# Performance work log

Hardware: AMD Instinct MI355X
Metric: run time of the kernel (lower is better)

Reference implementation:

```python
import jax, jax.numpy as jnp
import numpy as np

C = 96        # dim
HEADS = 8     # FrameHistoryRouter heads (StateAlignBlock forces heads=1)
WS = 4        # window_size = 2*scale_patchsize
NFC = 1       # num_frames_tocache
TOPK = 5
LOCAL_N = 4


def conv(x, w, stride=1, pad=0, groups=1):
    return jax.lax.conv_general_dilated(
        x, w, (stride, stride), [(pad, pad), (pad, pad)],
        dimension_numbers=("NCHW", "OIHW", "NCHW"), feature_group_count=groups)


def l2norm(x, axis):
    n = jnp.linalg.norm(x, axis=axis, keepdims=True)
    return x / jnp.maximum(n, 1e-12)


def setup_inputs() -> dict:
    key = jax.random.key(0)
    ks = jax.random.split(key, 16)
    def rn(i, shp, s=0.02):
        return jax.random.normal(ks[i], shp, dtype=jnp.float32) * s
    return {
        "x": jax.random.normal(ks[0], (2, C, 256, 256), dtype=jnp.float32),
        "sab_qk_w": rn(1, (2 * C, C, 1, 1)),
        "sab_qk_dw": rn(2, (2 * C, 1, 3, 3)),
        "sab_v_w": rn(3, (C, C, 1, 1)),
        "sab_v_dw": rn(4, (C, 1, 3, 3)),
        "sab_k2_w": rn(5, (2 * C, C, 1, 1)),
        "sab_k2_dw": rn(6, (2 * C, 1, WS, WS)),
        "sab_q2_w": rn(7, (2 * C, C, 1, 1)),
        "sab_q2_dw": rn(8, (2 * C, 1, WS, WS)),
        "sab_proj_w": rn(9, (C, C, 1, 1)),
        "sab_temp": jnp.ones((1, 1, 1), jnp.float32),
        "fhr_qkv_w": rn(10, (3 * C, C, 1, 1)),
        "fhr_qkv_dw": rn(11, (3 * C, 1, 3, 3)),
        "fhr_proj_w": rn(12, (C, C, 1, 1)),
        "fhr_temp": jnp.ones((HEADS, 1, 1), jnp.float32),
    }


def _forward(x, sab_qk_w, sab_qk_dw, sab_v_w, sab_v_dw, sab_k2_w, sab_k2_dw,
             sab_q2_w, sab_q2_dw, sab_proj_w, sab_temp,
             fhr_qkv_w, fhr_qkv_dw, fhr_proj_w, fhr_temp):
    b, c, h, w = x.shape
    # ---------- StateAlignBlock (no cache: first frame) ----------
    qk = conv(conv(x, sab_qk_w), sab_qk_dw, pad=1, groups=2 * c)
    q, k = jnp.split(qk, 2, axis=1)
    v = conv(conv(x, sab_v_w), sab_v_dw, pad=1, groups=c)
    k = conv(conv(k, sab_k2_w), sab_k2_dw, stride=WS, pad=1, groups=2 * c)
    q = conv(conv(q, sab_q2_w), sab_q2_dw, stride=WS, pad=1, groups=2 * c)
    H, W = q.shape[2], q.shape[3]            # = h//WS, w//WS
    N = H * W
    # b (1 d) h w -> b 1 1 (h w) d   with d = 2c
    q = q.reshape(b, 2 * c, N).transpose(0, 2, 1)[:, None, None]
    k = k.reshape(b, 2 * c, N).transpose(0, 2, 1)[:, None, None]
    # v: b (1 d) (p1 h) (p2 w) -> b 1 1 (h w) (p1 p2 d), p1=p2=WS, d=c
    h2, w2 = h // WS, w // WS
    v = v.reshape(b, c, WS, h2, WS, w2).transpose(0, 3, 5, 2, 4, 1)
    v = v.reshape(b, 1, 1, h2 * w2, WS * WS * c)
    q = l2norm(q, -1)
    k = l2norm(k, -1)
    attn = jnp.einsum("bfgnd,bfgmd->bfgnm", q, k) * sab_temp  # [b,1,1,N,N]
    # zero_out_non_top_k (top-5 along last dim; threshold form, ties negligible)
    kth = jax.lax.top_k(attn, TOPK)[0][..., TOPK - 1:TOPK]
    topk_mask = (attn >= kth).astype(attn.dtype)
    # local attention mask: manhattan distance <= LOCAL_N on the HxW patch grid
    yy, xx = jnp.meshgrid(jnp.arange(H), jnp.arange(W), indexing="ij")
    coords = jnp.stack([yy.ravel(), xx.ravel()], axis=-1)          # [N,2]
    dist = jnp.abs(coords[:, None, :] - coords[None, :, :]).sum(-1)
    local = (dist <= LOCAL_N).astype(attn.dtype)                   # [N,N]
    attn = attn * topk_mask + attn * local                         # as in torch
    # clipped_softmax
    zero = attn == 0
    s = jax.nn.softmax(jnp.where(zero, -jnp.inf, attn), axis=-1)
    s = jnp.where(zero, 0.0, s)
    s = s / s.sum(-1, keepdims=True)
    out = jnp.einsum("bfgnm,bfgmd->bfgnd", s, v)  # [b,1,1,N, WS*WS*c]
    F = 1  # curr_num_frames (no cache)
    # b f 1 (h w) (p1 p2 d) -> (b f) d (p1 h) (p2 w)
    out = out.reshape(b * F, h2, w2, WS, WS, c).transpose(0, 5, 3, 1, 4, 2)
    out = out.reshape(b * F, c, h, w)
    out = conv(out, sab_proj_w)
    aligned = out.reshape(b, F, c, h, w)
    k_s = k[:, -NFC:]  # [b,1,1,N,2c]
    v_s = v[:, -NFC:]
    # ---------- FrameHistoryRouter on aligned current frame ----------
    x2 = aligned[:, -1]
    qkv = conv(conv(x2, fhr_qkv_w), fhr_qkv_dw, pad=1, groups=3 * c)
    q2, k2, v2 = jnp.split(qkv, 3, axis=1)
    hd = c // HEADS
    q2 = q2.reshape(b, HEADS, hd, h * w)
    k2 = k2.reshape(b, HEADS, hd, h * w)
    v2 = v2.reshape(b, HEADS, hd, h * w)
    q2 = l2norm(q2, -1)
    k2 = l2norm(k2, -1)
    a2 = jnp.einsum("bhcn,bhdn->bhcd", q2, k2) * fhr_temp  # [b,H,hd,hd]
    a2 = jax.nn.softmax(a2, axis=-1)
    o2 = jnp.einsum("bhcd,bhdn->bhcn", a2, v2).reshape(b, c, h, w)
    o2 = conv(o2, fhr_proj_w)
    keep = int(NFC * c / HEADS)  # = hd
    return o2, k_s, v_s, k2[:, :, -keep:, :], v2[:, :, -keep:, :]


def reference(x, sab_qk_w, sab_qk_dw, sab_v_w, sab_v_dw, sab_k2_w, sab_k2_dw,
              sab_q2_w, sab_q2_dw, sab_proj_w, sab_temp,
              fhr_qkv_w, fhr_qkv_dw, fhr_proj_w, fhr_temp):
    return _forward(x, sab_qk_w, sab_qk_dw, sab_v_w, sab_v_dw, sab_k2_w,
                    sab_k2_dw, sab_q2_w, sab_q2_dw, sab_proj_w, sab_temp,
                    fhr_qkv_w, fhr_qkv_dw, fhr_proj_w, fhr_temp)
```

## Files before the change

kernel.cpp:

```cpp
#include <hip/hip_runtime.h>
#include <hip/hip_bf16.h>
#include <math.h>

#define HW 65536L

typedef __attribute__((ext_vector_type(8))) short bf16x8;
typedef __attribute__((ext_vector_type(4))) float f32x4;

__device__ __forceinline__ int iabs_(int v) { return v < 0 ? -v : v; }

__global__ __launch_bounds__(256) void wsplit(
    const float* __restrict__ qk, const float* __restrict__ v,
    const float* __restrict__ q2, const float* __restrict__ k2,
    const float* __restrict__ pj, const float* __restrict__ fq,
    const float* __restrict__ fp, unsigned short* __restrict__ whl)
{
  const int e = blockIdx.x*256 + threadIdx.x;
  if (e >= 110592) return;
  const int row = e / 96, col = e - row*96;
  float f;
  if      (row <  192) f = qk[e];
  else if (row <  288) f = v [(row-192)*96+col];
  else if (row <  480) f = q2[(row-288)*96+col];
  else if (row <  672) f = k2[(row-480)*96+col];
  else if (row <  768) f = pj[(row-672)*96+col];
  else if (row < 1056) f = fq[(row-768)*96+col];
  else                 f = fp[(row-1056)*96+col];
  __hip_bfloat16 h = __float2bfloat16(f);
  float hf = __bfloat162float(h);
  __hip_bfloat16 l = __float2bfloat16(f - hf);
  whl[e]          = *(unsigned short*)&h;
  whl[110592 + e] = *(unsigned short*)&l;
}

#define BLDS 104
__global__ __launch_bounds__(256) void conv1x1_mfma(
    const float* __restrict__ in, long in_bstride,
    const unsigned short* __restrict__ whl, int wrow0,
    float* __restrict__ out, long out_bstride,
    int mtiles, int mode)
{
  __shared__ unsigned short bhs[128*BLDS];
  __shared__ unsigned short bls[128*BLDS];
  const int t = threadIdx.x;
  const int p0 = blockIdx.x * 128;
  const int b = blockIdx.y;
  if (mode == 0) {
    #pragma unroll
    for (int it = 0; it < 12; it++) {
      const int idx = it*256 + t;
      const int g = idx >> 7;
      const int pix = idx & 127;
      const float* src = in + (long)b*in_bstride + (long)(g*4)*HW + p0 + pix;
      unsigned hh[4], ll[4];
      #pragma unroll
      for (int j = 0; j < 4; j++) {
        float f = src[(long)j*HW];
        unsigned u = __float_as_uint(f);
        hh[j] = u >> 16;
        float lof = f - __uint_as_float(u & 0xFFFF0000u);
        __hip_bfloat16 lb = __float2bfloat16(lof);
        ll[j] = *(unsigned short*)&lb;
      }
      uint2 hv, lv;
      hv.x = hh[0] | (hh[1] << 16); hv.y = hh[2] | (hh[3] << 16);
      lv.x = ll[0] | (ll[1] << 16); lv.y = ll[2] | (ll[3] << 16);
      *(uint2*)(bhs + pix*BLDS + g*4) = hv;
      *(uint2*)(bls + pix*BLDS + g*4) = lv;
    }
  } else {
    const int pp = t >> 1, half = (t & 1)*48;
    const int p = p0 + pp;
    const int py = p >> 8, px = p & 255;
    const float* src = in + (long)b*in_bstride
        + ((long)((py & 63)*64 + (px & 63))*16 + ((py >> 6)*4 + (px >> 6)))*96 + half;
    #pragma unroll
    for (int j4 = 0; j4 < 12; j4++) {
      float4 v4 = *(const float4*)&src[j4*4];
      float fv[4] = {v4.x, v4.y, v4.z, v4.w};
      unsigned hh[4], ll[4];
      #pragma unroll
      for (int u4 = 0; u4 < 4; u4++) {
        unsigned u = __float_as_uint(fv[u4]);
        hh[u4] = u >> 16;
        float lof = fv[u4] - __uint_as_float(u & 0xFFFF0000u);
        __hip_bfloat16 lb = __float2bfloat16(lof);
        ll[u4] = *(unsigned short*)&lb;
      }
      uint2 hv, lv;
      hv.x = hh[0] | (hh[1] << 16); hv.y = hh[2] | (hh[3] << 16);
      lv.x = ll[0] | (ll[1] << 16); lv.y = ll[2] | (ll[3] << 16);
      *(uint2*)(bhs + pp*BLDS + half + j4*4) = hv;
      *(uint2*)(bls + pp*BLDS + half + j4*4) = lv;
    }
  }
  __syncthreads();
  const int lane = t & 63, w = t >> 6;
  const int fr = lane & 15, fk = lane >> 4;
  bf16x8 Bh[2][3], Bl[2][3];
  #pragma unroll
  for (int nt = 0; nt < 2; nt++)
    #pragma unroll
    for (int kt = 0; kt < 3; kt++) {
      const int pix = w*32 + nt*16 + fr;
      Bh[nt][kt] = *(const bf16x8*)(bhs + pix*BLDS + kt*32 + fk*8);
      Bl[nt][kt] = *(const bf16x8*)(bls + pix*BLDS + kt*32 + fk*8);
    }
  float* dst = out + (long)b*out_bstride + p0 + w*32;
  for (int m = 0; m < mtiles; m++) {
    const long wbase = (long)(wrow0 + m*16 + fr)*96 + fk*8;
    bf16x8 Ah[3], Al[3];
    #pragma unroll
    for (int kt = 0; kt < 3; kt++) {
      Ah[kt] = *(const bf16x8*)(whl + wbase + kt*32);
      Al[kt] = *(const bf16x8*)(whl + 110592 + wbase + kt*32);
    }
    f32x4 acc[2] = {};
    #pragma unroll
    for (int nt = 0; nt < 2; nt++)
      #pragma unroll
      for (int kt = 0; kt < 3; kt++) {
        acc[nt] = __builtin_amdgcn_mfma_f32_16x16x32_bf16(Ah[kt], Bh[nt][kt], acc[nt], 0, 0, 0);
        acc[nt] = __builtin_amdgcn_mfma_f32_16x16x32_bf16(Ah[kt], Bl[nt][kt], acc[nt], 0, 0, 0);
        acc[nt] = __builtin_amdgcn_mfma_f32_16x16x32_bf16(Al[kt], Bh[nt][kt], acc[nt], 0, 0, 0);
      }
    #pragma unroll
    for (int nt = 0; nt < 2; nt++)
      #pragma unroll
      for (int r = 0; r < 4; r++)
        dst[(long)(m*16 + fk*4 + r)*HW + nt*16 + fr] = acc[nt][r];
  }
}

__global__ __launch_bounds__(256) void dw3x3v(
    const float* __restrict__ in, int inCH, const float* __restrict__ w,
    float* __restrict__ out, int outCH)
{
  const int t = threadIdx.x;
  const int p4 = blockIdx.x * 256 + t;
  const int ch = blockIdx.y, b = blockIdx.z;
  const int y = p4 >> 6, x0 = (p4 & 63) << 2;
  const float* ip = in + ((long)b*inCH + ch) * HW;
  const float* wp = w + ch*9;
  float a0 = 0.f, a1 = 0.f, a2 = 0.f, a3 = 0.f;
  #pragma unroll
  for (int dy = -1; dy <= 1; dy++) {
    const int yy = y + dy;
    if (yy < 0 || yy > 255) continue;
    const float* rp = ip + yy*256;
    const float4 c = *(const float4*)&rp[x0];
    const float left  = (x0 > 0)   ? rp[x0-1] : 0.f;
    const float right = (x0 < 252) ? rp[x0+4] : 0.f;
    const float w0 = wp[(dy+1)*3+0], w1 = wp[(dy+1)*3+1], w2 = wp[(dy+1)*3+2];
    a0 = fmaf(left, w0, a0); a0 = fmaf(c.x, w1, a0); a0 = fmaf(c.y, w2, a0);
    a1 = fmaf(c.x,  w0, a1); a1 = fmaf(c.y, w1, a1); a1 = fmaf(c.z, w2, a1);
    a2 = fmaf(c.y,  w0, a2); a2 = fmaf(c.z, w1, a2); a2 = fmaf(c.w, w2, a2);
    a3 = fmaf(c.z,  w0, a3); a3 = fmaf(c.w, w1, a3); a3 = fmaf(right, w2, a3);
  }
  float4 o; o.x = a0; o.y = a1; o.z = a2; o.w = a3;
  *(float4*)&out[((long)b*outCH + ch)*HW + y*256 + x0] = o;
}

__global__ __launch_bounds__(256) void dw3x3_vs(
    const float* __restrict__ in, const float* __restrict__ w,
    float* __restrict__ vs)
{
  __shared__ float tile[96*65];
  const int t = threadIdx.x;
  const int gb = blockIdx.x;
  const int b = blockIdx.y;
  const int y = gb >> 2, xb = gb & 3;
  #pragma unroll
  for (int i = 0; i < 6; i++) {
    const int idx = i*256 + t;
    const int ci = idx >> 4, q = idx & 15;
    const int x0 = xb*64 + q*4;
    const float* ip = in + ((long)b*96 + ci) * HW;
    const float* wp = w + ci*9;
    float a0 = 0.f, a1 = 0.f, a2 = 0.f, a3 = 0.f;
    #pragma unroll
    for (int dy = -1; dy <= 1; dy++) {
      const int yy = y + dy;
      if (yy < 0 || yy > 255) continue;
      const float* rp = ip + yy*256;
      const float4 c = *(const float4*)&rp[x0];
      const float left  = (x0 > 0)   ? rp[x0-1] : 0.f;
      const float right = (x0 < 252) ? rp[x0+4] : 0.f;
      const float w0 = wp[(dy+1)*3+0], w1 = wp[(dy+1)*3+1], w2 = wp[(dy+1)*3+2];
      a0 = fmaf(left, w0, a0); a0 = fmaf(c.x, w1, a0); a0 = fmaf(c.y, w2, a0);
      a1 = fmaf(c.x,  w0, a1); a1 = fmaf(c.y, w1, a1); a1 = fmaf(c.z, w2, a1);
      a2 = fmaf(c.y,  w0, a2); a2 = fmaf(c.z, w1, a2); a2 = fmaf(c.w, w2, a2);
      a3 = fmaf(c.z,  w0, a3); a3 = fmaf(c.w, w1, a3); a3 = fmaf(right, w2, a3);
    }
    const int xl = q*4;
    tile[ci*65 + xl    ] = a0;
    tile[ci*65 + xl + 1] = a1;
    tile[ci*65 + xl + 2] = a2;
    tile[ci*65 + xl + 3] = a3;
  }
  __syncthreads();
  const int blk = (y >> 6)*4 + xb;
  float* obase = vs + ((long)b*4096 + (long)(y & 63)*64) * 1536 + blk*96;
  #pragma unroll
  for (int i = 0; i < 24; i++) {
    const int idx = i*256 + t;
    const int nl = idx / 96, ci = idx % 96;
    obase[(long)nl*1536 + ci] = tile[ci*65 + nl];
  }
}

__global__ __launch_bounds__(256) void dw4x4s4(
    const float* __restrict__ in, const float* __restrict__ w,
    float* __restrict__ out)
{
  const int t = threadIdx.x;
  const int op = blockIdx.x * 256 + t;
  const int ch = blockIdx.y, b = blockIdx.z;
  const int oy = op >> 6, ox = op & 63;
  const float* ip = in + (long)(b*192 + ch) * HW;
  const float* wp = w + ch*16;
  float acc = 0.f;
  #pragma unroll
  for (int ty = 0; ty < 4; ty++) {
    int iy = 4*oy + ty - 1;
    if (iy < 0 || iy > 255) continue;
    #pragma unroll
    for (int tx = 0; tx < 4; tx++) {
      int ix = 4*ox + tx - 1;
      if (ix < 0 || ix > 255) continue;
      acc = fmaf(ip[iy*256 + ix], wp[ty*4 + tx], acc);
    }
  }
  out[(long)(b*192 + ch) * 4096 + op] = acc;
}

__global__ __launch_bounds__(256) void l2n192(
    const float* __restrict__ in, float* __restrict__ out)
{
  const int t = threadIdx.x;
  const int wid = t >> 6, lane = t & 63;
  const int gw = blockIdx.x * 4 + wid;
  const int b = gw >> 12, n = gw & 4095;
  const float* ip = in + (long)b * 786432;
  float v0 = ip[(long)(lane      ) * 4096 + n];
  float v1 = ip[(long)(lane +  64) * 4096 + n];
  float v2 = ip[(long)(lane + 128) * 4096 + n];
  float ss = v0*v0 + v1*v1 + v2*v2;
  #pragma unroll
  for (int s = 1; s < 64; s <<= 1) ss += __shfl_xor(ss, s, 64);
  float nrm = fmaxf(sqrtf(ss), 1e-12f);
  float* op = out + ((long)b*4096 + n) * 192;
  op[lane      ] = v0 / nrm;
  op[lane +  64] = v1 / nrm;
  op[lane + 128] = v2 / nrm;
}

__global__ __launch_bounds__(256) void bf16split(
    const float* __restrict__ in, unsigned short* __restrict__ outp)
{
  const int i = blockIdx.x * 256 + threadIdx.x;
  const int n = i / 192, k = i % 192;
  float f = in[i];
  __hip_bfloat16 h = __float2bfloat16(f);
  float hf = __bfloat162float(h);
  __hip_bfloat16 l = __float2bfloat16(f - hf);
  outp[(long)n*384 + k]       = *(unsigned short*)&h;
  outp[(long)n*384 + 192 + k] = *(unsigned short*)&l;
}

#define LDSROW 40
__global__ __launch_bounds__(256) void attn_qk_mfma(
    const unsigned short* __restrict__ Qsp, const unsigned short* __restrict__ Ksp,
    float* __restrict__ attn, const float* __restrict__ tp)
{
  __shared__ unsigned short qs[256*LDSROW];
  __shared__ unsigned short ks[256*LDSROW];
  const int t = threadIdx.x;
  const int lane = t & 63, w = t >> 6;
  const int n0 = blockIdx.x * 128;
  const int m0 = blockIdx.y * 128;
  const int wr = (w >> 1) * 64, wc = (w & 1) * 64;
  f32x4 acc[4][4] = {};
  const int srow = t & 127;
  const int shl  = t >> 7;
  const unsigned short* qsrc = Qsp + (long)(n0 + srow) * 384 + shl * 192;
  const unsigned short* ksrc = Ksp + (long)(m0 + srow) * 384 + shl * 192;
  unsigned short* qdst = qs + (shl*128 + srow) * LDSROW;
  unsigned short* kdst = ks + (shl*128 + srow) * LDSROW;
  const int fr = lane & 15;
  const int fk = lane >> 4;
  for (int s = 0; s < 6; s++) {
    __syncthreads();
    #pragma unroll
    for (int j = 0; j < 4; j++) {
      *(bf16x8*)(qdst + j*8) = *(const bf16x8*)(qsrc + s*32 + j*8);
      *(bf16x8*)(kdst + j*8) = *(const bf16x8*)(ksrc + s*32 + j*8);
    }
    __syncthreads();
    bf16x8 ah[4], al[4], bh[4], bl[4];
    #pragma unroll
    for (int i = 0; i < 4; i++) {
      ah[i] = *(const bf16x8*)(qs + (      wr + i*16 + fr) * LDSROW + fk*8);
      al[i] = *(const bf16x8*)(qs + (128 + wr + i*16 + fr) * LDSROW + fk*8);
      bh[i] = *(const bf16x8*)(ks + (      wc + i*16 + fr) * LDSROW + fk*8);
      bl[i] = *(const bf16x8*)(ks + (128 + wc + i*16 + fr) * LDSROW + fk*8);
    }
    #pragma unroll
    for (int i = 0; i < 4; i++)
      #pragma unroll
      for (int j = 0; j < 4; j++) {
        acc[i][j] = __builtin_amdgcn_mfma_f32_16x16x32_bf16(ah[i], bh[j], acc[i][j], 0, 0, 0);
        acc[i][j] = __builtin_amdgcn_mfma_f32_16x16x32_bf16(ah[i], bl[j], acc[i][j], 0, 0, 0);
        acc[i][j] = __builtin_amdgcn_mfma_f32_16x16x32_bf16(al[i], bh[j], acc[i][j], 0, 0, 0);
      }
  }
  const float temp = tp[0];
  #pragma unroll
  for (int i = 0; i < 4; i++)
    #pragma unroll
    for (int j = 0; j < 4; j++)
      #pragma unroll
      for (int r = 0; r < 4; r++) {
        const int nn = n0 + wr + i*16 + (lane >> 4)*4 + r;
        const int mm = m0 + wc + j*16 + (lane & 15);
        attn[(long)nn*4096 + mm] = acc[i][j][r] * temp;
      }
}

#define CAP 128
__global__ __launch_bounds__(256) void attn_out_k(
    const float* __restrict__ attn, const float* __restrict__ vs,
    float* __restrict__ outr)
{
  __shared__ float row[4096];
  __shared__ float top5[256*5];
  __shared__ int   lm[CAP];
  __shared__ float lw[CAP];
  __shared__ float ses[CAP];
  __shared__ float redf[8];
  __shared__ int   scan[256];
  const int t = threadIdx.x;
  const int n = blockIdx.x;
  const float* ar = attn + (long)n * 4096;
  #pragma unroll
  for (int k = 0; k < 16; k++) row[k*256 + t] = ar[k*256 + t];
  __syncthreads();
  float t0=-INFINITY,t1=-INFINITY,t2=-INFINITY,t3=-INFINITY,t4=-INFINITY;
  #pragma unroll
  for (int k = 0; k < 16; k++) {
    float v = row[k*256 + t];
    if (v > t4) {
      if (v > t0)      { t4=t3; t3=t2; t2=t1; t1=t0; t0=v; }
      else if (v > t1) { t4=t3; t3=t2; t2=t1; t1=v; }
      else if (v > t2) { t4=t3; t3=t2; t2=v; }
      else if (v > t3) { t4=t3; t3=v; }
      else             { t4=v; }
    }
  }
  top5[t*5+0]=t0; top5[t*5+1]=t1; top5[t*5+2]=t2; top5[t*5+3]=t3; top5[t*5+4]=t4;
  __syncthreads();
  for (int s = 128; s >= 1; s >>= 1) {
    if (t < s) {
      float* A = &top5[t*5];
      const float* B = &top5[(t+s)*5];
      float m[5]; int i = 0, j = 0;
      #pragma unroll
      for (int k = 0; k < 5; k++) {
        float av = A[i], bv = B[j];
        if (av >= bv) { m[k] = av; i++; } else { m[k] = bv; j++; }
      }
      #pragma unroll
      for (int k = 0; k < 5; k++) A[k] = m[k];
    }
    __syncthreads();
  }
  const float kth = top5[4];
  const int y = n >> 6, x = n & 63;
  int myc = 0;
  float wmax = -INFINITY;
  #pragma unroll
  for (int k = 0; k < 16; k++) {
    int m = k*256 + t;
    float a = row[m];
    int c = ((a >= kth) ? 1 : 0) +
            (((iabs_(y - (m >> 6)) + iabs_(x - (m & 63))) <= 4) ? 1 : 0);
    float wv = a * (float)c;
    if (wv != 0.0f) { myc++; wmax = fmaxf(wmax, wv); }
  }
  scan[t] = myc;
  __syncthreads();
  for (int s = 1; s < 256; s <<= 1) {
    int v = (t >= s) ? scan[t-s] : 0;
    __syncthreads();
    scan[t] += v;
    __syncthreads();
  }
  const int base = scan[t] - myc;
  const int cnt = scan[255];
  {
    int idx = base;
    #pragma unroll
    for (int k = 0; k < 16; k++) {
      int m = k*256 + t;
      float a = row[m];
      int c = ((a >= kth) ? 1 : 0) +
              (((iabs_(y - (m >> 6)) + iabs_(x - (m & 63))) <= 4) ? 1 : 0);
      float wv = a * (float)c;
      if (wv != 0.0f && idx < CAP) { lm[idx] = m; lw[idx] = wv; idx++; }
    }
  }
  #pragma unroll
  for (int s = 1; s < 64; s <<= 1) wmax = fmaxf(wmax, __shfl_xor(wmax, s, 64));
  if ((t & 63) == 0) redf[t >> 6] = wmax;
  __syncthreads();
  const float gmax = fmaxf(fmaxf(redf[0], redf[1]), fmaxf(redf[2], redf[3]));
  __syncthreads();
  if (t < cnt && t < CAP) ses[t] = expf(lw[t] - gmax);
  __syncthreads();
  float ps = (t < cnt && t < CAP) ? ses[t] : 0.f;
  #pragma unroll
  for (int s = 1; s < 64; s <<= 1) ps += __shfl_xor(ps, s, 64);
  if ((t & 63) == 0) redf[4 + (t >> 6)] = ps;
  __syncthreads();
  const float S = redf[4] + redf[5] + redf[6] + redf[7];
  const float invS = 1.0f / S;
  float a0=0,a1=0,a2=0,a3=0,a4=0,a5=0;
  const int ecnt = (cnt < CAP) ? cnt : CAP;
  for (int e = 0; e < ecnt; e++) {
    float se = ses[e] * invS;
    const float* vr = vs + (long)lm[e] * 1536;
    a0 = fmaf(se, vr[        t], a0);
    a1 = fmaf(se, vr[ 256 + t], a1);
    a2 = fmaf(se, vr[ 512 + t], a2);
    a3 = fmaf(se, vr[ 768 + t], a3);
    a4 = fmaf(se, vr[1024 + t], a4);
    a5 = fmaf(se, vr[1280 + t], a5);
  }
  float* orow = outr + (long)n * 1536;
  orow[        t] = a0;
  orow[ 256 + t] = a1;
  orow[ 512 + t] = a2;
  orow[ 768 + t] = a3;
  orow[1024 + t] = a4;
  orow[1280 + t] = a5;
}

__global__ __launch_bounds__(1024) void l2n_sp(
    const float* __restrict__ in, float* __restrict__ out)
{
  const int ch = blockIdx.x, b = blockIdx.y, t = threadIdx.x;
  const float* ip = in + ((long)b*96 + ch) * HW;
  float ss = 0.f;
  for (int i = t; i < 65536; i += 1024) { float v = ip[i]; ss = fmaf(v, v, ss); }
  __shared__ float red[16];
  #pragma unroll
  for (int s = 1; s < 64; s <<= 1) ss += __shfl_xor(ss, s, 64);
  if ((t & 63) == 0) red[t >> 6] = ss;
  __syncthreads();
  if (t == 0) {
    float s2 = 0.f;
    for (int i = 0; i < 16; i++) s2 += red[i];
    red[0] = fmaxf(sqrtf(s2), 1e-12f);
  }
  __syncthreads();
  const float nrm = red[0];
  float* op = out + ((long)b*96 + ch) * HW;
  for (int i = t; i < 65536; i += 1024) op[i] = ip[i] / nrm;
}

#define A2_NCH 16
__global__ __launch_bounds__(256) void a2_part(
    const float* __restrict__ q2n, const float* __restrict__ k2n,
    float* __restrict__ part)
{
  __shared__ float sh[24*260];
  const int t = threadIdx.x;
  const int ch = blockIdx.x, h = blockIdx.y, b = blockIdx.z;
  const long base = ((long)b*96 + h*12) * HW + ch*4096;
  const int c = t / 12, d = t - (t/12)*12;
  float acc = 0.f;
  for (int sub = 0; sub < 16; sub++) {
    __syncthreads();
    #pragma unroll
    for (int j = 0; j < 6; j++) {
      const int v = j*256 + t;
      const int row = v >> 6;
      const int col4 = v & 63;
      const float* src = (row < 12)
        ? q2n + base + (long)row*HW + sub*256 + col4*4
        : k2n + base + (long)(row-12)*HW + sub*256 + col4*4;
      *(float4*)&sh[row*260 + col4*4] = *(const float4*)src;
    }
    __syncthreads();
    if (t < 144) {
      const float* qr = &sh[c*260];
      const float* kr = &sh[(12+d)*260];
      #pragma unroll
      for (int i4 = 0; i4 < 64; i4++) {
        float4 qv = *(const float4*)&qr[i4*4];
        float4 kv = *(const float4*)&kr[i4*4];
        acc = fmaf(qv.x, kv.x, acc);
        acc = fmaf(qv.y, kv.y, acc);
        acc = fmaf(qv.z, kv.z, acc);
        acc = fmaf(qv.w, kv.w, acc);
      }
    }
  }
  if (t < 144)
    part[(((long)b*8 + h)*A2_NCH + ch)*144 + t] = acc;
}

__global__ __launch_bounds__(256) void a2_fin(
    const float* __restrict__ part, const float* __restrict__ temp,
    float* __restrict__ a2s)
{
  __shared__ float m[144];
  const int t = threadIdx.x;
  const int h = blockIdx.x, b = blockIdx.y;
  if (t < 144) {
    float s = 0.f;
    const float* pp = part + (((long)b*8 + h)*A2_NCH)*144 + t;
    #pragma unroll
    for (int ch = 0; ch < A2_NCH; ch++) s += pp[ch*144];
    m[t] = s * temp[h];
  }
  __syncthreads();
  if (t < 12) {
    float mx = -INFINITY;
    #pragma unroll
    for (int d = 0; d < 12; d++) mx = fmaxf(mx, m[t*12+d]);
    float e[12], sum = 0.f;
    #pragma unroll
    for (int d = 0; d < 12; d++) { e[d] = expf(m[t*12+d]-mx); sum += e[d]; }
    float inv = 1.0f/sum;
    float* op = a2s + (((long)b*8 + h)*12 + t)*12;
    #pragma unroll
    for (int d = 0; d < 12; d++) op[d] = e[d]*inv;
  }
}

__global__ __launch_bounds__(256) void o2pre_kern(
    const float* __restrict__ a2s, const float* __restrict__ v2,
    float* __restrict__ o2p)
{
  const int t = threadIdx.x;
  const int n = blockIdx.x * 256 + t;
  const int bh = blockIdx.y, b = bh >> 3, h = bh & 7;
  const float* a = a2s + (long)bh * 144;
  const float* vb = v2 + ((long)b*96 + h*12) * HW;
  float vv[12];
  #pragma unroll
  for (int d = 0; d < 12; d++) vv[d] = vb[(long)d*HW + n];
  float* ob = o2p + ((long)b*96 + h*12) * HW;
  #pragma unroll
  for (int c = 0; c < 12; c++) {
    float s = 0.f;
    #pragma unroll
    for (int d = 0; d < 12; d++) s = fmaf(a[c*12 + d], vv[d], s);
    ob[(long)c*HW + n] = s;
  }
}

extern "C" void kernel_launch(void* const* d_in, const int* in_sizes, int n_in,
                              void* d_out, int out_size, void* d_ws, size_t ws_size,
                              hipStream_t stream) {
  const float* x        = (const float*)d_in[0];
  const float* qk_w     = (const float*)d_in[1];
  const float* qk_dw    = (const float*)d_in[2];
  const float* v_w      = (const float*)d_in[3];
  const float* v_dw     = (const float*)d_in[4];
  const float* k2_w     = (const float*)d_in[5];
  const float* k2_dw    = (const float*)d_in[6];
  const float* q2_w     = (const float*)d_in[7];
  const float* q2_dw    = (const float*)d_in[8];
  const float* proj_w   = (const float*)d_in[9];
  const float* sab_temp = (const float*)d_in[10];
  const float* fqkv_w   = (const float*)d_in[11];
  const float* fqkv_dw  = (const float*)d_in[12];
  const float* fproj_w  = (const float*)d_in[13];
  const float* fhr_temp = (const float*)d_in[14];
  float* out = (float*)d_out;
  float* ws  = (float*)d_ws;

  float* O2  = out;
  float* KS  = out + 12582912;
  float* VS  = out + 14155776;
  float* K2N = out + 26738688;
  float* V2  = out + 39321600;

  float* A0   = ws;
  float* A1   = ws + 25165824;
  float* QD   = ws + 50331648;
  float* KD   = ws + 51904512;
  float* QN   = ws + 53477376;
  float* A2S  = ws + 55050240;
  float* PART = ws + 55052544;
  unsigned short* QSP = (unsigned short*)(A0 + 16777216);
  unsigned short* KSP = (unsigned short*)(A0 + 16777216 + 786432);
  unsigned short* WHL = (unsigned short*)QN;
  float* ALN = ws;
  float* PRE = ws + 12582912;
  float* OB  = ws + 12582912;

  dim3 b256(256), b1024(1024);

  wsplit<<<dim3(432), b256, 0, stream>>>(qk_w, v_w, q2_w, k2_w, proj_w, fqkv_w, fproj_w, WHL);
  conv1x1_mfma<<<dim3(512,2), b256, 0, stream>>>(x, 96L*HW, WHL, 0, A0, 192L*HW, 12, 0);
  dw3x3v<<<dim3(64,192,2), b256, 0, stream>>>(A0, 192, qk_dw, A1, 192);
  conv1x1_mfma<<<dim3(512,2), b256, 0, stream>>>(x, 96L*HW, WHL, 192, A0, 96L*HW, 6, 0);
  dw3x3_vs<<<dim3(1024,2), b256, 0, stream>>>(A0, v_dw, VS);
  conv1x1_mfma<<<dim3(512,2), b256, 0, stream>>>(A1, 192L*HW, WHL, 288, A0, 192L*HW, 12, 0);
  dw4x4s4<<<dim3(16,192,2), b256, 0, stream>>>(A0, q2_dw, QD);
  conv1x1_mfma<<<dim3(512,2), b256, 0, stream>>>(A1 + 96L*HW, 192L*HW, WHL, 480, A0, 192L*HW, 12, 0);
  dw4x4s4<<<dim3(16,192,2), b256, 0, stream>>>(A0, k2_dw, KD);
  l2n192<<<dim3(2048), b256, 0, stream>>>(QD, QN);
  l2n192<<<dim3(2048), b256, 0, stream>>>(KD, KS);
  for (int b = 0; b < 2; b++) {
    bf16split<<<dim3(3072), b256, 0, stream>>>(QN + (long)b*786432, QSP);
    bf16split<<<dim3(3072), b256, 0, stream>>>(KS + (long)b*786432, KSP);
    attn_qk_mfma<<<dim3(32,32), b256, 0, stream>>>(QSP, KSP, A0, sab_temp);
    attn_out_k<<<dim3(4096), b256, 0, stream>>>(
        A0, VS + (long)b*6291456, A1 + (long)b*6291456);
  }
  wsplit<<<dim3(432), b256, 0, stream>>>(qk_w, v_w, q2_w, k2_w, proj_w, fqkv_w, fproj_w, WHL);
  conv1x1_mfma<<<dim3(512,2), b256, 0, stream>>>(A1, 6291456L, WHL, 672, ALN, 96L*HW, 6, 1);
  conv1x1_mfma<<<dim3(512,2), b256, 0, stream>>>(ALN, 96L*HW, WHL, 768, PRE, 288L*HW, 18, 0);
  dw3x3v<<<dim3(64,96,2), b256, 0, stream>>>(PRE,            288, fqkv_dw,        ALN, 96);
  dw3x3v<<<dim3(64,96,2), b256, 0, stream>>>(PRE +  96L*HW, 288, fqkv_dw +  864, K2N, 96);
  dw3x3v<<<dim3(64,96,2), b256, 0, stream>>>(PRE + 192L*HW, 288, fqkv_dw + 1728, V2,  96);
  l2n_sp<<<dim3(96,2), b1024, 0, stream>>>(ALN, ALN);
  l2n_sp<<<dim3(96,2), b1024, 0, stream>>>(K2N, K2N);
  a2_part<<<dim3(A2_NCH,8,2), b256, 0, stream>>>(ALN, K2N, PART);
  a2_fin<<<dim3(8,2), b256, 0, stream>>>(PART, fhr_temp, A2S);
  o2pre_kern<<<dim3(256,16), b256, 0, stream>>>(A2S, V2, OB);
  conv1x1_mfma<<<dim3(512,2), b256, 0, stream>>>(OB, 96L*HW, WHL, 1056, O2, 96L*HW, 6, 0);
}
```

Measured before the change: 903.5 us.

## Vectorize strided depthwise conv, use wave-shuffle scan, fold q L2-norm into softmax

```diff
diff --git a/kernel.cpp b/kernel.cpp
--- a/kernel.cpp
+++ b/kernel.cpp
@@ -209,29 +209,38 @@
   }
 }
 
-__global__ __launch_bounds__(256) void dw4x4s4(
+__global__ __launch_bounds__(256) void dw4x4s4v(
     const float* __restrict__ in, const float* __restrict__ w,
     float* __restrict__ out)
 {
   const int t = threadIdx.x;
-  const int op = blockIdx.x * 256 + t;
+  const int p = blockIdx.x*256 + t;
   const int ch = blockIdx.y, b = blockIdx.z;
-  const int oy = op >> 6, ox = op & 63;
+  const int oy = p >> 4, qx = p & 15;
+  const int x0 = qx*16;
   const float* ip = in + (long)(b*192 + ch) * HW;
   const float* wp = w + ch*16;
-  float acc = 0.f;
+  float a0 = 0.f, a1 = 0.f, a2 = 0.f, a3 = 0.f;
   #pragma unroll
   for (int ty = 0; ty < 4; ty++) {
-    int iy = 4*oy + ty - 1;
+    const int iy = 4*oy + ty - 1;
     if (iy < 0 || iy > 255) continue;
-    #pragma unroll
-    for (int tx = 0; tx < 4; tx++) {
-      int ix = 4*ox + tx - 1;
-      if (ix < 0 || ix > 255) continue;
-      acc = fmaf(ip[iy*256 + ix], wp[ty*4 + tx], acc);
-    }
-  }
-  out[(long)(b*192 + ch) * 4096 + op] = acc;
+    const float* rp = ip + iy*256;
+    float r[17];
+    r[0] = (x0 > 0) ? rp[x0-1] : 0.f;
+    #pragma unroll
+    for (int k = 0; k < 4; k++) {
+      float4 v4 = *(const float4*)&rp[x0 + k*4];
+      r[1+k*4+0]=v4.x; r[1+k*4+1]=v4.y; r[1+k*4+2]=v4.z; r[1+k*4+3]=v4.w;
+    }
+    const float w0=wp[ty*4+0], w1=wp[ty*4+1], w2=wp[ty*4+2], w3=wp[ty*4+3];
+    a0=fmaf(r[ 0],w0,a0); a0=fmaf(r[ 1],w1,a0); a0=fmaf(r[ 2],w2,a0); a0=fmaf(r[ 3],w3,a0);
+    a1=fmaf(r[ 4],w0,a1); a1=fmaf(r[ 5],w1,a1); a1=fmaf(r[ 6],w2,a1); a1=fmaf(r[ 7],w3,a1);
+    a2=fmaf(r[ 8],w0,a2); a2=fmaf(r[ 9],w1,a2); a2=fmaf(r[10],w2,a2); a2=fmaf(r[11],w3,a2);
+    a3=fmaf(r[12],w0,a3); a3=fmaf(r[13],w1,a3); a3=fmaf(r[14],w2,a3); a3=fmaf(r[15],w3,a3);
+  }
+  float4 o; o.x=a0; o.y=a1; o.z=a2; o.w=a3;
+  *(float4*)&out[(long)(b*192 + ch)*4096 + oy*64 + qx*4] = o;
 }
 
 __global__ __launch_bounds__(256) void l2n192(
@@ -338,7 +347,7 @@
   __shared__ float lw[CAP];
   __shared__ float ses[CAP];
   __shared__ float redf[8];
-  __shared__ int   scan[256];
+  __shared__ int   wsum[4];
   const int t = threadIdx.x;
   const int n = blockIdx.x;
   const float* ar = attn + (long)n * 4096;
@@ -387,16 +396,19 @@
     float wv = a * (float)c;
     if (wv != 0.0f) { myc++; wmax = fmaxf(wmax, wv); }
   }
-  scan[t] = myc;
-  __syncthreads();
-  for (int s = 1; s < 256; s <<= 1) {
-    int v = (t >= s) ? scan[t-s] : 0;
-    __syncthreads();
-    scan[t] += v;
-    __syncthreads();
-  }
-  const int base = scan[t] - myc;
-  const int cnt = scan[255];
+  int inc = myc;
+  #pragma unroll
+  for (int s = 1; s < 64; s <<= 1) {
+    int v = __shfl_up(inc, s, 64);
+    if ((t & 63) >= s) inc += v;
+  }
+  if ((t & 63) == 63) wsum[t >> 6] = inc;
+  __syncthreads();
+  int pre = 0;
+  #pragma unroll
+  for (int wj = 0; wj < 4; wj++) pre += (wj < (t >> 6)) ? wsum[wj] : 0;
+  const int base = pre + inc - myc;
+  const int cnt = wsum[0] + wsum[1] + wsum[2] + wsum[3];
   {
     int idx = base;
     #pragma unroll
@@ -471,7 +483,7 @@
 #define A2_NCH 16
 __global__ __launch_bounds__(256) void a2_part(
     const float* __restrict__ q2n, const float* __restrict__ k2n,
-    float* __restrict__ part)
+    float* __restrict__ part, float* __restrict__ qqpart)
 {
   __shared__ float sh[24*260];
   const int t = threadIdx.x;
@@ -479,6 +491,7 @@
   const long base = ((long)b*96 + h*12) * HW + ch*4096;
   const int c = t / 12, d = t - (t/12)*12;
   float acc = 0.f;
+  float qq = 0.f;
   for (int sub = 0; sub < 16; sub++) {
     __syncthreads();
     #pragma unroll
@@ -504,17 +517,30 @@
         acc = fmaf(qv.z, kv.z, acc);
         acc = fmaf(qv.w, kv.w, acc);
       }
+    } else if (t < 156) {
+      const float* qr = &sh[(t-144)*260];
+      #pragma unroll
+      for (int i4 = 0; i4 < 64; i4++) {
+        float4 qv = *(const float4*)&qr[i4*4];
+        qq = fmaf(qv.x, qv.x, qq);
+        qq = fmaf(qv.y, qv.y, qq);
+        qq = fmaf(qv.z, qv.z, qq);
+        qq = fmaf(qv.w, qv.w, qq);
+      }
     }
   }
   if (t < 144)
     part[(((long)b*8 + h)*A2_NCH + ch)*144 + t] = acc;
+  else if (t < 156)
+    qqpart[(((long)b*8 + h)*A2_NCH + ch)*12 + (t-144)] = qq;
 }
 
 __global__ __launch_bounds__(256) void a2_fin(
-    const float* __restrict__ part, const float* __restrict__ temp,
-    float* __restrict__ a2s)
+    const float* __restrict__ part, const float* __restrict__ qqpart,
+    const float* __restrict__ temp, float* __restrict__ a2s)
 {
   __shared__ float m[144];
+  __shared__ float qn[12];
   const int t = threadIdx.x;
   const int h = blockIdx.x, b = blockIdx.y;
   if (t < 144) {
@@ -522,16 +548,25 @@
     const float* pp = part + (((long)b*8 + h)*A2_NCH)*144 + t;
     #pragma unroll
     for (int ch = 0; ch < A2_NCH; ch++) s += pp[ch*144];
-    m[t] = s * temp[h];
+    m[t] = s;
+  } else if (t < 156) {
+    float s = 0.f;
+    const float* pp = qqpart + (((long)b*8 + h)*A2_NCH)*12 + (t-144);
+    #pragma unroll
+    for (int ch = 0; ch < A2_NCH; ch++) s += pp[ch*12];
+    qn[t-144] = fmaxf(sqrtf(s), 1e-12f);
   }
   __syncthreads();
   if (t < 12) {
+    const float tv = temp[h];
+    const float scale = tv / qn[t];
     float mx = -INFINITY;
-    #pragma unroll
-    for (int d = 0; d < 12; d++) mx = fmaxf(mx, m[t*12+d]);
+    float a[12];
+    #pragma unroll
+    for (int d = 0; d < 12; d++) { a[d] = m[t*12+d] * scale; mx = fmaxf(mx, a[d]); }
     float e[12], sum = 0.f;
     #pragma unroll
-    for (int d = 0; d < 12; d++) { e[d] = expf(m[t*12+d]-mx); sum += e[d]; }
+    for (int d = 0; d < 12; d++) { e[d] = expf(a[d]-mx); sum += e[d]; }
     float inv = 1.0f/sum;
     float* op = a2s + (((long)b*8 + h)*12 + t)*12;
     #pragma unroll
@@ -601,6 +636,7 @@
   float* ALN = ws;
   float* PRE = ws + 12582912;
   float* OB  = ws + 12582912;
+  float* QQP = QD;
 
   dim3 b256(256), b1024(1024);
 
@@ -610,9 +646,9 @@
   conv1x1_mfma<<<dim3(512,2), b256, 0, stream>>>(x, 96L*HW, WHL, 192, A0, 96L*HW, 6, 0);
   dw3x3_vs<<<dim3(1024,2), b256, 0, stream>>>(A0, v_dw, VS);
   conv1x1_mfma<<<dim3(512,2), b256, 0, stream>>>(A1, 192L*HW, WHL, 288, A0, 192L*HW, 12, 0);
-  dw4x4s4<<<dim3(16,192,2), b256, 0, stream>>>(A0, q2_dw, QD);
+  dw4x4s4v<<<dim3(4,192,2), b256, 0, stream>>>(A0, q2_dw, QD);
   conv1x1_mfma<<<dim3(512,2), b256, 0, stream>>>(A1 + 96L*HW, 192L*HW, WHL, 480, A0, 192L*HW, 12, 0);
-  dw4x4s4<<<dim3(16,192,2), b256, 0, stream>>>(A0, k2_dw, KD);
+  dw4x4s4v<<<dim3(4,192,2), b256, 0, stream>>>(A0, k2_dw, KD);
   l2n192<<<dim3(2048), b256, 0, stream>>>(QD, QN);
   l2n192<<<dim3(2048), b256, 0, stream>>>(KD, KS);
   for (int b = 0; b < 2; b++) {
@@ -628,10 +664,9 @@
   dw3x3v<<<dim3(64,96,2), b256, 0, stream>>>(PRE,            288, fqkv_dw,        ALN, 96);
   dw3x3v<<<dim3(64,96,2), b256, 0, stream>>>(PRE +  96L*HW, 288, fqkv_dw +  864, K2N, 96);
   dw3x3v<<<dim3(64,96,2), b256, 0, stream>>>(PRE + 192L*HW, 288, fqkv_dw + 1728, V2,  96);
-  l2n_sp<<<dim3(96,2), b1024, 0, stream>>>(ALN, ALN);
   l2n_sp<<<dim3(96,2), b1024, 0, stream>>>(K2N, K2N);
-  a2_part<<<dim3(A2_NCH,8,2), b256, 0, stream>>>(ALN, K2N, PART);
-  a2_fin<<<dim3(8,2), b256, 0, stream>>>(PART, fhr_temp, A2S);
+  a2_part<<<dim3(A2_NCH,8,2), b256, 0, stream>>>(ALN, K2N, PART, QQP);
+  a2_fin<<<dim3(8,2), b256, 0, stream>>>(PART, QQP, fhr_temp, A2S);
   o2pre_kern<<<dim3(256,16), b256, 0, stream>>>(A2S, V2, OB);
   conv1x1_mfma<<<dim3(512,2), b256, 0, stream>>>(OB, 96L*HW, WHL, 1056, O2, 96L*HW, 6, 0);
 }
```

New measurement: 897.6 us. No clear change (-0.7%).
